# Optimization experiments

Hardware: AMD Instinct MI355X
Metric: run time of the kernel (lower is better)

Reference implementation:

```python
import jax, jax.numpy as jnp
import numpy as np

K = 9          # neighbors = conv1d kernel = stride
OUT_CH = 64


def setup_inputs() -> dict:
    key = jax.random.key(0)
    k1, k2 = jax.random.split(key)
    x = jax.random.normal(k1, (8, 32, 56, 56), dtype=jnp.float32)
    W = jax.random.normal(k2, (OUT_CH, 32, K), dtype=jnp.float32) * 0.05  # conv1d weight (O,I,K), no bias
    return {"x": x, "W": W}


def reference(x, W):
    B, C, H, Wd = x.shape
    T = H * Wd
    xf = x.reshape(B, C, T)                                   # flatten spatial dims
    # cosine similarity matrix (F.normalize with eps=1e-12)
    nrm = jnp.sqrt(jnp.sum(xf * xf, axis=1, keepdims=True))
    xn = xf / jnp.maximum(nrm, 1e-12)
    sim = jnp.einsum('bct,bcs->bts', xn, xn)                  # [B,T,T]
    sim = jnp.clip(sim, -1.0, 1.0)
    sim = jnp.where(jnp.eye(T, dtype=bool)[None], 1.1, sim)   # self always top-1
    # top-K largest, then sort indices ascending (as in torch code)
    _, idx = jax.lax.top_k(sim, K)                            # [B,T,K]
    idx = jnp.sort(idx, axis=-1)
    # gather neighbor features: prime[b,c,t,k] = xf[b,c,idx[b,t,k]]
    prime = jax.vmap(lambda xb, ib: xb[:, ib])(xf, idx)       # [B,C,T,K]
    prime = prime.reshape(B, C, T * K)
    # conv1d kernel=K stride=K, no bias -> length T
    out = jax.lax.conv_general_dilated(
        prime, W, window_strides=(K,), padding='VALID',
        dimension_numbers=('NCH', 'OIH', 'NCH'))              # [B,OUT_CH,T]
    return out.reshape(B, OUT_CH, H, Wd)
```

## Files before the change

kernel.cpp:

```cpp
#include <hip/hip_runtime.h>
#include <stdint.h>
#include <math.h>

#define BB 8
#define CC 32
#define TT 3136
#define KK 9
#define OC 64

#define NEGINF (-3.0e38f)

__global__ __launch_bounds__(256) void norm_kernel(
    const float* __restrict__ x, float* __restrict__ xnT,
    float* __restrict__ xfT, double* __restrict__ invn)
{
    int t = blockIdx.x * 256 + threadIdx.x;
    int b = blockIdx.y;
    if (t >= TT) return;
    const float* xp = x + (size_t)b * CC * TT + t;
    float v[CC];
    double ss = 0.0;
#pragma unroll
    for (int c = 0; c < CC; ++c) {
        v[c] = xp[(size_t)c * TT];
        ss = fma((double)v[c], (double)v[c], ss);
    }
    double inv = 1.0 / fmax(sqrt(ss), 1e-12);
    invn[(size_t)b * TT + t] = inv;
    float invf = (float)inv;
    float* pf = xfT + ((size_t)b * TT + t) * CC;
    float* pn = xnT + ((size_t)b * TT + t) * CC;
#pragma unroll
    for (int c = 0; c < CC; c += 4) {
        *(float4*)(pf + c) = make_float4(v[c], v[c+1], v[c+2], v[c+3]);
        *(float4*)(pn + c) = make_float4(v[c]*invf, v[c+1]*invf, v[c+2]*invf, v[c+3]*invf);
    }
}

__device__ __forceinline__ void insert12(float (&val)[12], int (&ids)[12],
                                         float s, int idx)
{
#pragma unroll
    for (int j = 11; j >= 1; --j) {
        bool up   = s > val[j-1];
        bool here = (s > val[j]) && !up;
        val[j] = up ? val[j-1] : (here ? s   : val[j]);
        ids[j] = up ? ids[j-1] : (here ? idx : ids[j]);
    }
    if (s > val[0]) { val[0] = s; ids[0] = idx; }
}

__device__ __forceinline__ void insert12_u64(uint64_t (&kv)[12], uint64_t k)
{
#pragma unroll
    for (int j = 11; j >= 1; --j) {
        bool up   = k > kv[j-1];
        bool here = (k > kv[j]) && !up;
        kv[j] = up ? kv[j-1] : (here ? k : kv[j]);
    }
    if (k > kv[0]) kv[0] = k;
}

template<int JN>
__device__ __forceinline__ void scan_tile(
    const float* __restrict__ cols, const float (&rv)[CC],
    float (&val)[12], int (&ids)[12], int q, int t, int s0)
{
    float sc[JN];
#pragma unroll
    for (int j = 0; j < JN; ++j) sc[j] = 0.f;

#pragma unroll
    for (int c = 0; c < CC; c += 4) {
        float rx = rv[c], ry = rv[c+1], rz = rv[c+2], rw = rv[c+3];
#pragma unroll
        for (int j = 0; j < JN; ++j) {
            float4 cv = *(const float4*)(cols + (j*8 + q)*36 + c);
            sc[j] = fmaf(rx, cv.x, sc[j]);
            sc[j] = fmaf(ry, cv.y, sc[j]);
            sc[j] = fmaf(rz, cv.z, sc[j]);
            sc[j] = fmaf(rw, cv.w, sc[j]);
        }
    }
#pragma unroll
    for (int j = 0; j < JN; ++j)
        if (s0 + j*8 + q == t) sc[j] = NEGINF;

    for (int pass = 0; pass < JN; ++pass) {
        float m = sc[0]; int am = 0;
#pragma unroll
        for (int j = 1; j < JN; ++j) {
            bool g = sc[j] > m;
            m  = g ? sc[j] : m;
            am = g ? j : am;
        }
        bool want = m > val[11];
        if (!__any(want)) break;
        if (want) {
            insert12(val, ids, m, s0 + am*8 + q);
#pragma unroll
            for (int j = 0; j < JN; ++j)
                if (am == j) sc[j] = NEGINF;
        }
    }
}

__global__ __launch_bounds__(256) void topk_kernel(
    const float* __restrict__ xnT, const float* __restrict__ xfT,
    const double* __restrict__ invn, int* __restrict__ idxo)
{
    __shared__ uint64_t mbuf[32 * 97];
    float* cols = (float*)mbuf;

    int tid = threadIdx.x;
    int b   = blockIdx.y;
    int r   = tid >> 3;
    int q   = tid & 7;
    int t   = blockIdx.x * 32 + r;

    const float* rowp = xnT + ((size_t)b * TT + t) * CC;
    float rv[CC];
#pragma unroll
    for (int c = 0; c < CC; c += 4) {
        float4 f = *(const float4*)(rowp + c);
        rv[c] = f.x; rv[c+1] = f.y; rv[c+2] = f.z; rv[c+3] = f.w;
    }

    float val[12]; int ids[12];
#pragma unroll
    for (int j = 0; j < 12; ++j) { val[j] = NEGINF; ids[j] = 0x7FFFFFFF; }

    for (int s0 = 0; s0 < TT; s0 += 128) {
        int count = min(128, TT - s0);
        __syncthreads();
        for (int f = tid; f < count * 8; f += 256) {
            int col = f >> 3, part = f & 7;
            *(float4*)(cols + col*36 + part*4) =
                *(const float4*)(xnT + ((size_t)b * TT + s0 + col) * CC + part*4);
        }
        __syncthreads();
        if (count == 128) scan_tile<16>(cols, rv, val, ids, q, t, s0);
        else              scan_tile<8> (cols, rv, val, ids, q, t, s0);
    }
    __syncthreads();

#pragma unroll
    for (int j = 0; j < 12; ++j) {
        uint32_t u = __float_as_uint(val[j]);
        u = (u & 0x80000000u) ? ~u : (u | 0x80000000u);
        mbuf[r*97 + q*12 + j] = ((uint64_t)u << 32) | (uint64_t)(~(uint32_t)ids[j]);
    }
    __syncthreads();

    if (q == 0) {
        uint64_t kv[12];
#pragma unroll
        for (int j = 0; j < 12; ++j) kv[j] = 0ull;
        for (int i = 0; i < 96; ++i) {
            uint64_t k = mbuf[r*97 + i];
            if (k > kv[11]) insert12_u64(kv, k);
        }

        const float* rawp = xfT + ((size_t)b * TT + t) * CC;
#pragma unroll
        for (int c = 0; c < CC; c += 4) {
            float4 f = *(const float4*)(rawp + c);
            rv[c] = f.x; rv[c+1] = f.y; rv[c+2] = f.z; rv[c+3] = f.w;
        }

        double v8[8]; int i8[8];
#pragma unroll
        for (int j = 0; j < 8; ++j) { v8[j] = -1.0e300; i8[j] = 0x7FFFFFFF; }
        for (int jc = 0; jc < 12; ++jc) {
            int idx = (int)(~(uint32_t)kv[jc]);
            const float* cp = xfT + ((size_t)b * TT + idx) * CC;
            double acc = 0.0;
#pragma unroll
            for (int c = 0; c < CC; ++c)
                acc = fma((double)rv[c], (double)cp[c], acc);
            double scr = acc * invn[(size_t)b * TT + idx];

            bool better7 = (scr > v8[7]) || (scr == v8[7] && idx < i8[7]);
            if (better7) {
#pragma unroll
                for (int j = 7; j >= 1; --j) {
                    bool up   = (scr > v8[j-1]) || (scr == v8[j-1] && idx < i8[j-1]);
                    bool here = ((scr > v8[j]) || (scr == v8[j] && idx < i8[j])) && !up;
                    v8[j] = up ? v8[j-1] : (here ? scr : v8[j]);
                    i8[j] = up ? i8[j-1] : (here ? idx : i8[j]);
                }
                bool top = (scr > v8[0]) || (scr == v8[0] && idx < i8[0]);
                if (top) { v8[0] = scr; i8[0] = idx; }
            }
        }

        int oi[9];
#pragma unroll
        for (int j = 0; j < 8; ++j) oi[j] = i8[j];
        oi[8] = t;
        for (int a = 1; a < 9; ++a) {
            int kvv = oi[a]; int jj = a - 1;
            while (jj >= 0 && oi[jj] > kvv) { oi[jj+1] = oi[jj]; --jj; }
            oi[jj+1] = kvv;
        }
        int* op = idxo + ((size_t)b * TT + t) * KK;
#pragma unroll
        for (int m = 0; m < 9; ++m) op[m] = oi[m];
    }
}

__global__ __launch_bounds__(256) void gconv_kernel(
    const float* __restrict__ xfT, const int* __restrict__ idxi,
    const float* __restrict__ Wt, float* __restrict__ out)
{
    __shared__ float wl[288 * 65];
    __shared__ float ot[4][64 * 17];

    int tid = threadIdx.x;
    int b   = blockIdx.y;
    int t0  = blockIdx.x * 64;

    for (int f = tid; f < OC * 288; f += 256) {
        int o  = f / 288;
        int ck = f - o * 288;
        wl[ck * 65 + o] = Wt[f];
    }
    __syncthreads();

    int w    = tid >> 6;
    int lane = tid & 63;
    int tw0  = t0 + w * 16;

    for (int i = 0; i < 16; ++i) {
        int t = tw0 + i;
        const int* ip = idxi + ((size_t)b * TT + t) * KK;
        float acc = 0.f;
#pragma unroll
        for (int k = 0; k < KK; ++k) {
            int s = __builtin_amdgcn_readfirstlane(ip[k]);
            const float* col = xfT + ((size_t)b * TT + s) * CC;
#pragma unroll
            for (int c4 = 0; c4 < CC; c4 += 4) {
                float4 xv = *(const float4*)(col + c4);
                acc = fmaf(xv.x, wl[((c4+0)*9 + k)*65 + lane], acc);
                acc = fmaf(xv.y, wl[((c4+1)*9 + k)*65 + lane], acc);
                acc = fmaf(xv.z, wl[((c4+2)*9 + k)*65 + lane], acc);
                acc = fmaf(xv.w, wl[((c4+3)*9 + k)*65 + lane], acc);
            }
        }
        ot[w][lane * 17 + i] = acc;
    }
    __syncthreads();

    for (int j = 0; j < 16; ++j) {
        int fl = j * 64 + lane;
        int o  = fl >> 4;
        int ii = fl & 15;
        out[((size_t)b * OC + o) * TT + tw0 + ii] = ot[w][o * 17 + ii];
    }
}

extern "C" void kernel_launch(void* const* d_in, const int* in_sizes, int n_in,
                              void* d_out, int out_size, void* d_ws, size_t ws_size,
                              hipStream_t stream)
{
    const float* x  = (const float*)d_in[0];
    const float* Wt = (const float*)d_in[1];
    float* out = (float*)d_out;

    float*  xnT  = (float*)d_ws;
    float*  xfT  = xnT + (size_t)BB * TT * CC;
    double* invn = (double*)(xfT + (size_t)BB * TT * CC);
    int*    idw  = (int*)(invn + (size_t)BB * TT);

    dim3 g1((TT + 255) / 256, BB);
    norm_kernel<<<g1, 256, 0, stream>>>(x, xnT, xfT, invn);

    dim3 g2(TT / 32, BB);
    topk_kernel<<<g2, 256, 0, stream>>>(xnT, xfT, invn, idw);

    dim3 g3(TT / 64, BB);
    gconv_kernel<<<g3, 256, 0, stream>>>(xfT, idw, Wt, out);
}
```

Before: 539.6 us.

## Replace per-thread top-k insertion with two-pass threshold selection and register-tiled similarity

```diff
diff --git a/kernel.cpp b/kernel.cpp
--- a/kernel.cpp
+++ b/kernel.cpp
@@ -9,6 +9,22 @@
 #define OC 64
 
 #define NEGINF (-3.0e38f)
+#define BR 32
+#define RT 4
+#define MT 8
+#define BC 256
+#define NTILE 13
+#define CAP 56
+#define EPS 1e-4f
+
+__device__ __forceinline__ uint32_t f2s(float v) {
+    uint32_t u = __float_as_uint(v);
+    return (u & 0x80000000u) ? ~u : (u | 0x80000000u);
+}
+__device__ __forceinline__ float s2f(uint32_t u) {
+    u = (u & 0x80000000u) ? (u & 0x7FFFFFFFu) : ~u;
+    return __uint_as_float(u);
+}
 
 __global__ __launch_bounds__(256) void norm_kernel(
     const float* __restrict__ x, float* __restrict__ xnT,
@@ -37,173 +53,215 @@
     }
 }
 
-__device__ __forceinline__ void insert12(float (&val)[12], int (&ids)[12],
-                                         float s, int idx)
-{
-#pragma unroll
-    for (int j = 11; j >= 1; --j) {
-        bool up   = s > val[j-1];
-        bool here = (s > val[j]) && !up;
-        val[j] = up ? val[j-1] : (here ? s   : val[j]);
-        ids[j] = up ? ids[j-1] : (here ? idx : ids[j]);
-    }
-    if (s > val[0]) { val[0] = s; ids[0] = idx; }
-}
-
-__device__ __forceinline__ void insert12_u64(uint64_t (&kv)[12], uint64_t k)
-{
-#pragma unroll
-    for (int j = 11; j >= 1; --j) {
-        bool up   = k > kv[j-1];
-        bool here = (k > kv[j]) && !up;
-        kv[j] = up ? kv[j-1] : (here ? k : kv[j]);
-    }
-    if (k > kv[0]) kv[0] = k;
-}
-
-template<int JN>
-__device__ __forceinline__ void scan_tile(
-    const float* __restrict__ cols, const float (&rv)[CC],
-    float (&val)[12], int (&ids)[12], int q, int t, int s0)
-{
-    float sc[JN];
-#pragma unroll
-    for (int j = 0; j < JN; ++j) sc[j] = 0.f;
-
-#pragma unroll
-    for (int c = 0; c < CC; c += 4) {
-        float rx = rv[c], ry = rv[c+1], rz = rv[c+2], rw = rv[c+3];
-#pragma unroll
-        for (int j = 0; j < JN; ++j) {
-            float4 cv = *(const float4*)(cols + (j*8 + q)*36 + c);
-            sc[j] = fmaf(rx, cv.x, sc[j]);
-            sc[j] = fmaf(ry, cv.y, sc[j]);
-            sc[j] = fmaf(rz, cv.z, sc[j]);
-            sc[j] = fmaf(rw, cv.w, sc[j]);
-        }
-    }
-#pragma unroll
-    for (int j = 0; j < JN; ++j)
-        if (s0 + j*8 + q == t) sc[j] = NEGINF;
-
-    for (int pass = 0; pass < JN; ++pass) {
-        float m = sc[0]; int am = 0;
-#pragma unroll
-        for (int j = 1; j < JN; ++j) {
-            bool g = sc[j] > m;
-            m  = g ? sc[j] : m;
-            am = g ? j : am;
-        }
-        bool want = m > val[11];
-        if (!__any(want)) break;
-        if (want) {
-            insert12(val, ids, m, s0 + am*8 + q);
-#pragma unroll
-            for (int j = 0; j < JN; ++j)
-                if (am == j) sc[j] = NEGINF;
-        }
-    }
-}
-
 __global__ __launch_bounds__(256) void topk_kernel(
     const float* __restrict__ xnT, const float* __restrict__ xfT,
     const double* __restrict__ invn, int* __restrict__ idxo)
 {
-    __shared__ uint64_t mbuf[32 * 97];
-    float* cols = (float*)mbuf;
-
-    int tid = threadIdx.x;
-    int b   = blockIdx.y;
-    int r   = tid >> 3;
-    int q   = tid & 7;
-    int t   = blockIdx.x * 32 + r;
-
-    const float* rowp = xnT + ((size_t)b * TT + t) * CC;
-    float rv[CC];
-#pragma unroll
-    for (int c = 0; c < CC; c += 4) {
-        float4 f = *(const float4*)(rowp + c);
-        rv[c] = f.x; rv[c+1] = f.y; rv[c+2] = f.z; rv[c+3] = f.w;
-    }
-
-    float val[12]; int ids[12];
-#pragma unroll
-    for (int j = 0; j < 12; ++j) { val[j] = NEGINF; ids[j] = 0x7FFFFFFF; }
-
-    for (int s0 = 0; s0 < TT; s0 += 128) {
-        int count = min(128, TT - s0);
+    __shared__ __align__(16) float colbuf[BC * 36];
+    __shared__ __align__(16) float rowbuf[BR * 36];
+    __shared__ int candidx[BR * CAP];
+    __shared__ int cnt[BR];
+
+    int tid   = threadIdx.x;
+    int b     = blockIdx.y;
+    int browg = blockIdx.x * BR;
+    size_t bbase = (size_t)b * TT;
+
+    int ig = tid >> 5;
+    int j  = tid & 31;
+
+    {
+        int row = tid >> 3, part = tid & 7;
+        *(float4*)&rowbuf[row * 36 + part * 4] =
+            *(const float4*)&xnT[(bbase + browg + row) * CC + part * 4];
+    }
+    if (tid < BR) cnt[tid] = 0;
+
+    float acc[RT][MT];
+
+    float mseg[RT];
+#pragma unroll
+    for (int r = 0; r < RT; ++r) mseg[r] = NEGINF;
+
+    for (int tt = 0; tt < NTILE; ++tt) {
+        int ct0 = tt * BC;
+        int ccn = (ct0 + BC <= TT) ? BC : (TT - ct0);
+        int mm  = ccn >> 5;
         __syncthreads();
-        for (int f = tid; f < count * 8; f += 256) {
-            int col = f >> 3, part = f & 7;
-            *(float4*)(cols + col*36 + part*4) =
-                *(const float4*)(xnT + ((size_t)b * TT + s0 + col) * CC + part*4);
+        for (int g = tid; g < ccn * 8; g += 256) {
+            int col = g >> 3, part = g & 7;
+            *(float4*)&colbuf[col * 36 + part * 4] =
+                *(const float4*)&xnT[(bbase + ct0 + col) * CC + part * 4];
         }
         __syncthreads();
-        if (count == 128) scan_tile<16>(cols, rv, val, ids, q, t, s0);
-        else              scan_tile<8> (cols, rv, val, ids, q, t, s0);
+
+#pragma unroll
+        for (int r = 0; r < RT; ++r)
+#pragma unroll
+            for (int m = 0; m < MT; ++m) acc[r][m] = 0.f;
+#pragma unroll
+        for (int cq = 0; cq < 8; ++cq) {
+            float4 a[RT];
+#pragma unroll
+            for (int r = 0; r < RT; ++r)
+                a[r] = *(const float4*)&rowbuf[(ig*RT + r) * 36 + cq * 4];
+#pragma unroll
+            for (int m = 0; m < MT; ++m) {
+                float4 bv = *(const float4*)&colbuf[(j + 32*m) * 36 + cq * 4];
+#pragma unroll
+                for (int r = 0; r < RT; ++r) {
+                    acc[r][m] = fmaf(a[r].x, bv.x, acc[r][m]);
+                    acc[r][m] = fmaf(a[r].y, bv.y, acc[r][m]);
+                    acc[r][m] = fmaf(a[r].z, bv.z, acc[r][m]);
+                    acc[r][m] = fmaf(a[r].w, bv.w, acc[r][m]);
+                }
+            }
+        }
+
+#pragma unroll
+        for (int r = 0; r < RT; ++r) {
+            int rowg = browg + ig*RT + r;
+#pragma unroll
+            for (int m = 0; m < MT; ++m) {
+                int col = ct0 + j + 32*m;
+                float v = (col == rowg) ? NEGINF : acc[r][m];
+                if (m < mm) mseg[r] = fmaxf(mseg[r], v);
+            }
+        }
+    }
+
+    int lane = tid & 63;
+    unsigned long long halfmask = 0xFFFFFFFFull << (lane & 32);
+    float th[RT];
+#pragma unroll
+    for (int r = 0; r < RT; ++r) {
+        uint32_t key = f2s(mseg[r]);
+        uint32_t nth = 0;
+        for (int round = 0; round < 9; ++round) {
+            uint32_t m = key;
+#pragma unroll
+            for (int d = 1; d < 32; d <<= 1) {
+                uint32_t o = (uint32_t)__shfl_xor((int)m, d, 64);
+                m = (o > m) ? o : m;
+            }
+            nth = m;
+            unsigned long long bal = __ballot(key == m) & halfmask;
+            int leader = __ffsll(bal) - 1;
+            if (lane == leader) key = 0;
+        }
+        th[r] = s2f(nth) - EPS;
+    }
+
+    for (int tt = 0; tt < NTILE; ++tt) {
+        int ct0 = tt * BC;
+        int ccn = (ct0 + BC <= TT) ? BC : (TT - ct0);
+        int mm  = ccn >> 5;
+        __syncthreads();
+        for (int g = tid; g < ccn * 8; g += 256) {
+            int col = g >> 3, part = g & 7;
+            *(float4*)&colbuf[col * 36 + part * 4] =
+                *(const float4*)&xnT[(bbase + ct0 + col) * CC + part * 4];
+        }
+        __syncthreads();
+
+#pragma unroll
+        for (int r = 0; r < RT; ++r)
+#pragma unroll
+            for (int m = 0; m < MT; ++m) acc[r][m] = 0.f;
+#pragma unroll
+        for (int cq = 0; cq < 8; ++cq) {
+            float4 a[RT];
+#pragma unroll
+            for (int r = 0; r < RT; ++r)
+                a[r] = *(const float4*)&rowbuf[(ig*RT + r) * 36 + cq * 4];
+#pragma unroll
+            for (int m = 0; m < MT; ++m) {
+                float4 bv = *(const float4*)&colbuf[(j + 32*m) * 36 + cq * 4];
+#pragma unroll
+                for (int r = 0; r < RT; ++r) {
+                    acc[r][m] = fmaf(a[r].x, bv.x, acc[r][m]);
+                    acc[r][m] = fmaf(a[r].y, bv.y, acc[r][m]);
+                    acc[r][m] = fmaf(a[r].z, bv.z, acc[r][m]);
+                    acc[r][m] = fmaf(a[r].w, bv.w, acc[r][m]);
+                }
+            }
+        }
+
+#pragma unroll
+        for (int r = 0; r < RT; ++r) {
+            int rowl = ig*RT + r;
+            int rowg = browg + rowl;
+#pragma unroll
+            for (int m = 0; m < MT; ++m) {
+                int col = ct0 + j + 32*m;
+                float v = (col == rowg) ? NEGINF : acc[r][m];
+                if (m < mm && v >= th[r]) {
+                    int n = atomicAdd(&cnt[rowl], 1);
+                    if (n < CAP) candidx[rowl * CAP + n] = col;
+                }
+            }
+        }
     }
     __syncthreads();
 
-#pragma unroll
-    for (int j = 0; j < 12; ++j) {
-        uint32_t u = __float_as_uint(val[j]);
-        u = (u & 0x80000000u) ? ~u : (u | 0x80000000u);
-        mbuf[r*97 + q*12 + j] = ((uint64_t)u << 32) | (uint64_t)(~(uint32_t)ids[j]);
+    double* scorebuf = (double*)colbuf;
+    for (int g = tid; g < BR * CAP; g += 256) {
+        int row  = g / CAP;
+        int slot = g - row * CAP;
+        int n = min(cnt[row], CAP);
+        if (slot < n) {
+            int s = candidx[row * CAP + slot];
+            const float* xt = xfT + (bbase + browg + row) * CC;
+            const float* xs = xfT + (bbase + s) * CC;
+            double a2 = 0.0;
+#pragma unroll
+            for (int c = 0; c < CC; c += 4) {
+                float4 xtv = *(const float4*)(xt + c);
+                float4 xsv = *(const float4*)(xs + c);
+                a2 = fma((double)xtv.x, (double)xsv.x, a2);
+                a2 = fma((double)xtv.y, (double)xsv.y, a2);
+                a2 = fma((double)xtv.z, (double)xsv.z, a2);
+                a2 = fma((double)xtv.w, (double)xsv.w, a2);
+            }
+            scorebuf[row * CAP + slot] = a2 * invn[bbase + s];
+        }
     }
     __syncthreads();
 
-    if (q == 0) {
-        uint64_t kv[12];
-#pragma unroll
-        for (int j = 0; j < 12; ++j) kv[j] = 0ull;
-        for (int i = 0; i < 96; ++i) {
-            uint64_t k = mbuf[r*97 + i];
-            if (k > kv[11]) insert12_u64(kv, k);
-        }
-
-        const float* rawp = xfT + ((size_t)b * TT + t) * CC;
-#pragma unroll
-        for (int c = 0; c < CC; c += 4) {
-            float4 f = *(const float4*)(rawp + c);
-            rv[c] = f.x; rv[c+1] = f.y; rv[c+2] = f.z; rv[c+3] = f.w;
-        }
-
+    if ((tid & 7) == 0) {
+        int row = tid >> 3;
+        int t   = browg + row;
+        int n   = min(cnt[row], CAP);
         double v8[8]; int i8[8];
 #pragma unroll
-        for (int j = 0; j < 8; ++j) { v8[j] = -1.0e300; i8[j] = 0x7FFFFFFF; }
-        for (int jc = 0; jc < 12; ++jc) {
-            int idx = (int)(~(uint32_t)kv[jc]);
-            const float* cp = xfT + ((size_t)b * TT + idx) * CC;
-            double acc = 0.0;
-#pragma unroll
-            for (int c = 0; c < CC; ++c)
-                acc = fma((double)rv[c], (double)cp[c], acc);
-            double scr = acc * invn[(size_t)b * TT + idx];
-
+        for (int jj = 0; jj < 8; ++jj) { v8[jj] = -1.0e300; i8[jj] = 0x7FFFFFFF; }
+        for (int sl = 0; sl < n; ++sl) {
+            double scr = scorebuf[row * CAP + sl];
+            int    idx = candidx[row * CAP + sl];
             bool better7 = (scr > v8[7]) || (scr == v8[7] && idx < i8[7]);
             if (better7) {
 #pragma unroll
-                for (int j = 7; j >= 1; --j) {
-                    bool up   = (scr > v8[j-1]) || (scr == v8[j-1] && idx < i8[j-1]);
-                    bool here = ((scr > v8[j]) || (scr == v8[j] && idx < i8[j])) && !up;
-                    v8[j] = up ? v8[j-1] : (here ? scr : v8[j]);
-                    i8[j] = up ? i8[j-1] : (here ? idx : i8[j]);
+                for (int jj = 7; jj >= 1; --jj) {
+                    bool up   = (scr > v8[jj-1]) || (scr == v8[jj-1] && idx < i8[jj-1]);
+                    bool here = ((scr > v8[jj]) || (scr == v8[jj] && idx < i8[jj])) && !up;
+                    v8[jj] = up ? v8[jj-1] : (here ? scr : v8[jj]);
+                    i8[jj] = up ? i8[jj-1] : (here ? idx : i8[jj]);
                 }
                 bool top = (scr > v8[0]) || (scr == v8[0] && idx < i8[0]);
                 if (top) { v8[0] = scr; i8[0] = idx; }
             }
         }
-
         int oi[9];
 #pragma unroll
-        for (int j = 0; j < 8; ++j) oi[j] = i8[j];
+        for (int jj = 0; jj < 8; ++jj)
+            oi[jj] = (i8[jj] == 0x7FFFFFFF) ? t : i8[jj];
         oi[8] = t;
         for (int a = 1; a < 9; ++a) {
-            int kvv = oi[a]; int jj = a - 1;
-            while (jj >= 0 && oi[jj] > kvv) { oi[jj+1] = oi[jj]; --jj; }
-            oi[jj+1] = kvv;
-        }
-        int* op = idxo + ((size_t)b * TT + t) * KK;
+            int kv = oi[a]; int jj = a - 1;
+            while (jj >= 0 && oi[jj] > kv) { oi[jj+1] = oi[jj]; --jj; }
+            oi[jj+1] = kv;
+        }
+        int* op = idxo + (bbase + t) * KK;
 #pragma unroll
         for (int m = 0; m < 9; ++m) op[m] = oi[m];
     }
@@ -219,6 +277,7 @@
     int tid = threadIdx.x;
     int b   = blockIdx.y;
     int t0  = blockIdx.x * 64;
+    size_t bbase = (size_t)b * TT;
 
     for (int f = tid; f < OC * 288; f += 256) {
         int o  = f / 288;
@@ -231,29 +290,48 @@
     int lane = tid & 63;
     int tw0  = t0 + w * 16;
 
-    for (int i = 0; i < 16; ++i) {
-        int t = tw0 + i;
-        const int* ip = idxi + ((size_t)b * TT + t) * KK;
-        float acc = 0.f;
+    for (int i0 = 0; i0 < 16; i0 += 4) {
+        float a0 = 0.f, a1 = 0.f, a2 = 0.f, a3 = 0.f;
+        const int* ip0 = idxi + (bbase + tw0 + i0) * KK;
 #pragma unroll
         for (int k = 0; k < KK; ++k) {
-            int s = __builtin_amdgcn_readfirstlane(ip[k]);
-            const float* col = xfT + ((size_t)b * TT + s) * CC;
-#pragma unroll
-            for (int c4 = 0; c4 < CC; c4 += 4) {
-                float4 xv = *(const float4*)(col + c4);
-                acc = fmaf(xv.x, wl[((c4+0)*9 + k)*65 + lane], acc);
-                acc = fmaf(xv.y, wl[((c4+1)*9 + k)*65 + lane], acc);
-                acc = fmaf(xv.z, wl[((c4+2)*9 + k)*65 + lane], acc);
-                acc = fmaf(xv.w, wl[((c4+3)*9 + k)*65 + lane], acc);
-            }
-        }
-        ot[w][lane * 17 + i] = acc;
+            int s0 = __builtin_amdgcn_readfirstlane(ip0[0*KK + k]);
+            int s1 = __builtin_amdgcn_readfirstlane(ip0[1*KK + k]);
+            int s2 = __builtin_amdgcn_readfirstlane(ip0[2*KK + k]);
+            int s3 = __builtin_amdgcn_readfirstlane(ip0[3*KK + k]);
+            const float* c0 = xfT + (bbase + s0) * CC;
+            const float* c1 = xfT + (bbase + s1) * CC;
+            const float* c2 = xfT + (bbase + s2) * CC;
+            const float* c3 = xfT + (bbase + s3) * CC;
+#pragma unroll
+            for (int c4 = 0; c4 < 8; ++c4) {
+                float4 x0 = *(const float4*)(c0 + c4*4);
+                float4 x1 = *(const float4*)(c1 + c4*4);
+                float4 x2 = *(const float4*)(c2 + c4*4);
+                float4 x3 = *(const float4*)(c3 + c4*4);
+                float w0 = wl[((c4*4+0)*9 + k)*65 + lane];
+                float w1 = wl[((c4*4+1)*9 + k)*65 + lane];
+                float w2 = wl[((c4*4+2)*9 + k)*65 + lane];
+                float w3 = wl[((c4*4+3)*9 + k)*65 + lane];
+                a0 = fmaf(x0.x, w0, a0); a0 = fmaf(x0.y, w1, a0);
+                a0 = fmaf(x0.z, w2, a0); a0 = fmaf(x0.w, w3, a0);
+                a1 = fmaf(x1.x, w0, a1); a1 = fmaf(x1.y, w1, a1);
+                a1 = fmaf(x1.z, w2, a1); a1 = fmaf(x1.w, w3, a1);
+                a2 = fmaf(x2.x, w0, a2); a2 = fmaf(x2.y, w1, a2);
+                a2 = fmaf(x2.z, w2, a2); a2 = fmaf(x2.w, w3, a2);
+                a3 = fmaf(x3.x, w0, a3); a3 = fmaf(x3.y, w1, a3);
+                a3 = fmaf(x3.z, w2, a3); a3 = fmaf(x3.w, w3, a3);
+            }
+        }
+        ot[w][lane * 17 + i0 + 0] = a0;
+        ot[w][lane * 17 + i0 + 1] = a1;
+        ot[w][lane * 17 + i0 + 2] = a2;
+        ot[w][lane * 17 + i0 + 3] = a3;
     }
     __syncthreads();
 
-    for (int j = 0; j < 16; ++j) {
-        int fl = j * 64 + lane;
+    for (int jj = 0; jj < 16; ++jj) {
+        int fl = jj * 64 + lane;
         int o  = fl >> 4;
         int ii = fl & 15;
         out[((size_t)b * OC + o) * TT + tw0 + ii] = ot[w][o * 17 + ii];
@@ -276,7 +354,7 @@
     dim3 g1((TT + 255) / 256, BB);
     norm_kernel<<<g1, 256, 0, stream>>>(x, xnT, xfT, invn);
 
-    dim3 g2(TT / 32, BB);
+    dim3 g2(TT / BR, BB);
     topk_kernel<<<g2, 256, 0, stream>>>(xnT, xfT, invn, idw);
 
     dim3 g3(TT / 64, BB);
```

After: 1.190 ms. +120.4%, slower.
